# Kernel optimization log

Measured on AMD Instinct MI355X. Metric: run time of the kernel, lower is better.

## Reference

```python
import jax, jax.numpy as jnp
import numpy as np

H = 512      # hidden_size
V = 50257    # vocab_size
B = 64       # batch
T = 512      # sequence length


def setup_inputs() -> dict:
    key = jax.random.key(0)
    k1, k2, k3, k4 = jax.random.split(key, 4)
    # Parameters as constructed in HMM.__init__ (row-stochastic / log-normalized)
    alpha_exp = jax.nn.softmax(jax.random.normal(k1, (H, H), dtype=jnp.float32), axis=-1)
    beta = jax.nn.log_softmax(jax.random.normal(k2, (H, V), dtype=jnp.float32), axis=-1)
    gamma_exp = jax.nn.softmax(jax.random.normal(k3, (1, H), dtype=jnp.float32), axis=-1)
    input_ids = jax.random.randint(k4, (B, T), 0, V)
    return {"alpha_exp": alpha_exp, "beta": beta, "gamma_exp": gamma_exp, "input_ids": input_ids}


def _stable_mvm(log_W, log_x):
    # log-space matvec: log(W @ x) with max-shift stabilization (matches torch stable_mvm)
    x_max = jnp.max(log_x)
    x = jnp.exp(log_x - x_max)                       # (H,)
    w_max = jnp.max(log_W, axis=1, keepdims=True)    # (H,1)
    W = jnp.exp(log_W - w_max)                       # (H,H)
    z = W @ x                                        # (H,)
    return jnp.log(z) + x_max + jnp.squeeze(w_max, -1)


def reference(alpha_exp, beta, gamma_exp, input_ids):
    # HMM.compute_forward_probability
    logA_T = jnp.log(alpha_exp + 1e-12).T            # (H,H) transposed transition log-probs
    alpha0 = jnp.log(gamma_exp) + beta[:, input_ids[:, 0]].T   # (B,H)
    mvm = jax.vmap(_stable_mvm, in_axes=(None, 0))

    def step(alpha_prev, x_t):
        a = mvm(logA_T, alpha_prev) + beta[:, x_t].T  # (B,H)
        return a, None

    alpha_final, _ = jax.lax.scan(step, alpha0, input_ids[:, 1:].T)
    return alpha_final
```

## Files before the change

kernel.cpp:

```cpp
#include <hip/hip_runtime.h>
#include <hip/hip_bf16.h>

#define HH 512
#define VV 50257
#define TL 512
#define NT 512
#define DYN_LDS 98304

typedef __attribute__((ext_vector_type(4))) float floatx4;
typedef __attribute__((ext_vector_type(8))) int intx8;

__device__ __forceinline__ unsigned short f2bf(float f) {
  union { float f; unsigned int u; } v; v.f = f;
  unsigned int r = (v.u + 0x7fffu + ((v.u >> 16) & 1u)) >> 16;
  return (unsigned short)r;
}
__device__ __forceinline__ float bf2f(unsigned short h) {
  union { unsigned int u; float f; } v; v.u = ((unsigned int)h) << 16;
  return v.f;
}

__device__ __forceinline__ float wave_max_dpp(float x) {
  int xi = __builtin_bit_cast(int, x);
#define DPPSTEP(ctrl)                                                              \
  {                                                                                \
    int yi = __builtin_amdgcn_update_dpp(xi, xi, (ctrl), 0xf, 0xf, false);         \
    float a = __builtin_bit_cast(float, xi), b = __builtin_bit_cast(float, yi);    \
    xi = __builtin_bit_cast(int, fmaxf(a, b));                                     \
  }
  DPPSTEP(0xB1)
  DPPSTEP(0x4E)
  DPPSTEP(0x141)
  DPPSTEP(0x140)
  DPPSTEP(0x142)
  DPPSTEP(0x143)
#undef DPPSTEP
  return __builtin_bit_cast(float, __builtin_amdgcn_readlane(xi, 63));
}

__global__ void colmaxK(const float* __restrict__ A, float* __restrict__ cmax) {
  __shared__ float red[4][64];
  int x = threadIdx.x & 63;
  int y = threadIdx.x >> 6;
  int c = blockIdx.x * 64 + x;
  float m = -INFINITY;
  for (int j = y; j < HH; j += 4) m = fmaxf(m, A[j * HH + c]);
  red[y][x] = m;
  __syncthreads();
  if (y == 0)
    cmax[c] = fmaxf(fmaxf(red[0][x], red[1][x]), fmaxf(red[2][x], red[3][x])) + 1e-12f;
}

__global__ void buildWf8sK(const float* __restrict__ A, const float* __restrict__ cmax,
                           intx8* __restrict__ Wf8s) {
  int gid = blockIdx.x * 256 + threadIdx.x;
  int L = gid & 63, r = gid >> 6;
  int kk = r & 3, T = r >> 2;
  int n = T * 16 + (L & 15);
  int kbase = kk * 128 + (L >> 4) * 32;
  float inv = 1.0f / cmax[n];
  intx8 o;
#pragma unroll
  for (int d = 0; d < 8; ++d) {
    float v0 = (A[(kbase + 4 * d + 0) * HH + n] + 1e-12f) * inv;
    float v1 = (A[(kbase + 4 * d + 1) * HH + n] + 1e-12f) * inv;
    float v2 = (A[(kbase + 4 * d + 2) * HH + n] + 1e-12f) * inv;
    float v3 = (A[(kbase + 4 * d + 3) * HH + n] + 1e-12f) * inv;
    unsigned pk;
    asm("v_cvt_pk_fp8_f32 %0, %1, %2" : "=v"(pk) : "v"(v0), "v"(v1));
    asm("v_cvt_pk_fp8_f32 %0, %1, %2 op_sel:[0,0,1]" : "+v"(pk) : "v"(v2), "v"(v3));
    o[d] = (int)pk;
  }
  Wf8s[gid] = o;
}

__global__ void buildPtab(const float* __restrict__ beta, const float* __restrict__ cmax,
                          unsigned short* __restrict__ Ptab) {
  __shared__ float tile[32][33];
  int v0 = blockIdx.x * 32, h0 = blockIdx.y * 32;
  int tx = threadIdx.x, ty = threadIdx.y;
#pragma unroll
  for (int k = 0; k < 4; ++k) {
    int v = v0 + tx;
    if (v < VV) tile[ty + 8 * k][tx] = beta[(h0 + ty + 8 * k) * VV + v];
  }
  __syncthreads();
  float cm = cmax[h0 + tx];
#pragma unroll
  for (int k = 0; k < 4; ++k) {
    int v = v0 + ty + 8 * k;
    if (v < VV) Ptab[(long)v * HH + h0 + tx] = f2bf(__expf(tile[tx][ty + 8 * k]) * cm);
  }
}

__global__ __launch_bounds__(NT, 2) __attribute__((amdgpu_waves_per_eu(2, 2)))
void hmm_main(const intx8* __restrict__ Wf8s,
              const unsigned short* __restrict__ Ptab,
              const float* __restrict__ gamma,
              const float* __restrict__ cmax,
              const int* __restrict__ ids,
              float* __restrict__ out) {
  extern __shared__ char dls[];
  unsigned char* xbuf = (unsigned char*)dls;
  int* elds = (int*)(dls + 1024);
  int* ids_l = (int*)(dls + 1088);

  const int b = blockIdx.x, tid = threadIdx.x;
  const int w = tid >> 6, L = tid & 63;
  const int q = L >> 4;
  const long bT = (long)b * TL;

  ids_l[tid] = ids[bT + tid];

  intx8 wa[4][4];
#pragma unroll
  for (int tau = 0; tau < 4; ++tau)
#pragma unroll
    for (int kk = 0; kk < 4; ++kk)
      wa[tau][kk] = Wf8s[((4 * w + tau) * 4 + kk) * 64 + L];

  const int n = tid;
  float A = 0.f;

  {
    const int id0 = ids[bT];
    float u0 = gamma[n] * bf2f(Ptab[(long)id0 * HH + n]) / cmax[n];
    float m = wave_max_dpp(u0);
    int ebits = (__builtin_bit_cast(int, m) >> 23) & 0xFF;
    float nf = __builtin_bit_cast(float, (254 - ebits) << 23);
    float x0 = u0 * nf;
    unsigned pk;
    asm("v_cvt_pk_fp8_f32 %0, %1, %2" : "=v"(pk) : "v"(x0), "v"(x0));
    xbuf[n] = (unsigned char)(pk & 0xff);
    if (L == 0) elds[w] = ebits - 127;
    __syncthreads();
  }

  unsigned short pvc = Ptab[(long)ids_l[1] * HH + n];

  for (int t = 1; t < TL; ++t) {
    const int idn = ids_l[(t + 1 < TL) ? (t + 1) : t];
    const unsigned short pvn = Ptab[(long)idn * HH + n];

    const int pr = (t - 1) & 1;
    const unsigned char* xb = xbuf + pr * 512;

    int4 ea = *(const int4*)&elds[pr * 8];
    int4 eb = *(const int4*)&elds[pr * 8 + 4];
    int E = max(max(max(ea.x, ea.y), max(ea.z, ea.w)),
                max(max(eb.x, eb.y), max(eb.z, eb.w)));
    A += (float)E * 0.69314718056f;
    const int s0 = max(127 + ea.x - E, 0), s1 = max(127 + ea.y - E, 0);
    const int s2 = max(127 + ea.z - E, 0), s3 = max(127 + ea.w - E, 0);
    const int s4 = max(127 + eb.x - E, 0), s5 = max(127 + eb.y - E, 0);
    const int s6 = max(127 + eb.z - E, 0), s7 = max(127 + eb.w - E, 0);
    const int sa0 = s0 * 0x0101 + s1 * 0x01010000;
    const int sa1 = s2 * 0x0101 + s3 * 0x01010000;
    const int sa2 = s4 * 0x0101 + s5 * 0x01010000;
    const int sa3 = s6 * 0x0101 + s7 * 0x01010000;

    intx8 af0 = *(const intx8*)(xb + 0 * 128 + q * 32);
    intx8 af1 = *(const intx8*)(xb + 1 * 128 + q * 32);
    intx8 af2 = *(const intx8*)(xb + 2 * 128 + q * 32);
    intx8 af3 = *(const intx8*)(xb + 3 * 128 + q * 32);

    floatx4 acc[4];
#pragma unroll
    for (int tau = 0; tau < 4; ++tau) acc[tau] = (floatx4){0.f, 0.f, 0.f, 0.f};

    __builtin_amdgcn_s_setprio(1);
#pragma unroll
    for (int tau = 0; tau < 4; ++tau) {
      acc[tau] = __builtin_amdgcn_mfma_scale_f32_16x16x128_f8f6f4(
          af0, wa[tau][0], acc[tau], 0, 0, 0, sa0, 0, 0x7F7F7F7F);
      acc[tau] = __builtin_amdgcn_mfma_scale_f32_16x16x128_f8f6f4(
          af1, wa[tau][1], acc[tau], 0, 0, 0, sa1, 0, 0x7F7F7F7F);
      acc[tau] = __builtin_amdgcn_mfma_scale_f32_16x16x128_f8f6f4(
          af2, wa[tau][2], acc[tau], 0, 0, 0, sa2, 0, 0x7F7F7F7F);
      acc[tau] = __builtin_amdgcn_mfma_scale_f32_16x16x128_f8f6f4(
          af3, wa[tau][3], acc[tau], 0, 0, 0, sa3, 0, 0x7F7F7F7F);
    }
    __builtin_amdgcn_s_setprio(0);

    const float z = (q < 2) ? (q == 0 ? acc[0][0] : acc[1][0])
                            : (q == 2 ? acc[2][0] : acc[3][0]);
    const float un = z * bf2f(pvc);

    if (t == TL - 1) {
      out[(long)b * HH + n] = __logf(fmaxf(un, 1e-37f)) + A;
    } else {
      float m = wave_max_dpp(un);
      int ebits = (__builtin_bit_cast(int, m) >> 23) & 0xFF;
      float nf = __builtin_bit_cast(float, (254 - ebits) << 23);
      float x = un * nf;
      unsigned pk;
      asm("v_cvt_pk_fp8_f32 %0, %1, %2" : "=v"(pk) : "v"(x), "v"(x));
      xbuf[(t & 1) * 512 + n] = (unsigned char)(pk & 0xff);
      if (L == 0) elds[(t & 1) * 8 + w] = ebits - 127;
      asm volatile("s_waitcnt lgkmcnt(0)" ::: "memory");
      __builtin_amdgcn_s_barrier();
      __builtin_amdgcn_sched_barrier(0);
    }
    pvc = pvn;
  }
}

extern "C" void kernel_launch(void* const* d_in, const int* in_sizes, int n_in,
                              void* d_out, int out_size, void* d_ws, size_t ws_size,
                              hipStream_t stream) {
  const float* alpha_exp = (const float*)d_in[0];
  const float* beta = (const float*)d_in[1];
  const float* gamma = (const float*)d_in[2];
  const int* ids = (const int*)d_in[3];
  float* out = (float*)d_out;

  char* ws = (char*)d_ws;
  float* cmax = (float*)(ws + 0);
  intx8* Wf8s = (intx8*)(ws + 4096);
  unsigned short* Ptab = (unsigned short*)(ws + 528384);

  (void)hipFuncSetAttribute((const void*)hmm_main,
                            hipFuncAttributeMaxDynamicSharedMemorySize, DYN_LDS);

  colmaxK<<<8, 256, 0, stream>>>(alpha_exp, cmax);
  buildWf8sK<<<32, 256, 0, stream>>>(alpha_exp, cmax, Wf8s);
  dim3 gT((VV + 31) / 32, HH / 32), bTd(32, 8);
  buildPtab<<<gT, bTd, 0, stream>>>(beta, cmax, Ptab);

  hmm_main<<<64, NT, DYN_LDS, stream>>>(Wf8s, Ptab, gamma, cmax, ids, out);
}
```

Before: 623.9 us.

## Halve workgroup to four waves, each computing two output columns per step

Shrinks the per-batch workgroup from 8 waves to 4, so each wave holds twice as many fp8 weight tiles in registers (8x4 intx8) and each lane produces two hidden states per timestep. Per-wave exponents are stored as bytes and packed into one dword, which simplifies the scale computation. The intent is to cut barrier cost and cross-wave exponent reduction in the serial recurrence. In exchange, each wave issues twice as many MFMAs per step on the critical path, and register pressure rises sharply with one wave per EU.

```diff
diff --git a/kernel.cpp b/kernel.cpp
--- a/kernel.cpp
+++ b/kernel.cpp
@@ -4,7 +4,7 @@
 #define HH 512
 #define VV 50257
 #define TL 512
-#define NT 512
+#define NT 256
 #define DYN_LDS 98304
 
 typedef __attribute__((ext_vector_type(4))) float floatx4;
@@ -93,7 +93,7 @@
   }
 }
 
-__global__ __launch_bounds__(NT, 2) __attribute__((amdgpu_waves_per_eu(2, 2)))
+__global__ __launch_bounds__(NT, 1) __attribute__((amdgpu_waves_per_eu(1, 1)))
 void hmm_main(const intx8* __restrict__ Wf8s,
               const unsigned short* __restrict__ Ptab,
               const float* __restrict__ gamma,
@@ -102,106 +102,118 @@
               float* __restrict__ out) {
   extern __shared__ char dls[];
   unsigned char* xbuf = (unsigned char*)dls;
-  int* elds = (int*)(dls + 1024);
-  int* ids_l = (int*)(dls + 1088);
+  unsigned char* eldsb = (unsigned char*)(dls + 1024);
+  int* ids_l = (int*)(dls + 1040);
 
   const int b = blockIdx.x, tid = threadIdx.x;
   const int w = tid >> 6, L = tid & 63;
-  const int q = L >> 4;
+  const int q = L >> 4, l16 = L & 15;
   const long bT = (long)b * TL;
 
   ids_l[tid] = ids[bT + tid];
-
-  intx8 wa[4][4];
-#pragma unroll
-  for (int tau = 0; tau < 4; ++tau)
+  ids_l[tid + 256] = ids[bT + tid + 256];
+
+  intx8 wa[8][4];
+#pragma unroll
+  for (int tau = 0; tau < 8; ++tau)
 #pragma unroll
     for (int kk = 0; kk < 4; ++kk)
-      wa[tau][kk] = Wf8s[((4 * w + tau) * 4 + kk) * 64 + L];
-
-  const int n = tid;
+      wa[tau][kk] = Wf8s[((8 * w + tau) * 4 + kk) * 64 + L];
+
+  const int n0 = 128 * w + 32 * q + l16;
+  const int n1 = n0 + 16;
+
   float A = 0.f;
 
   {
     const int id0 = ids[bT];
-    float u0 = gamma[n] * bf2f(Ptab[(long)id0 * HH + n]) / cmax[n];
-    float m = wave_max_dpp(u0);
+    float u0 = gamma[n0] * bf2f(Ptab[(long)id0 * HH + n0]) / cmax[n0];
+    float u1 = gamma[n1] * bf2f(Ptab[(long)id0 * HH + n1]) / cmax[n1];
+    float m = wave_max_dpp(fmaxf(u0, u1));
     int ebits = (__builtin_bit_cast(int, m) >> 23) & 0xFF;
     float nf = __builtin_bit_cast(float, (254 - ebits) << 23);
-    float x0 = u0 * nf;
+    float x0 = u0 * nf, x1 = u1 * nf;
     unsigned pk;
-    asm("v_cvt_pk_fp8_f32 %0, %1, %2" : "=v"(pk) : "v"(x0), "v"(x0));
-    xbuf[n] = (unsigned char)(pk & 0xff);
-    if (L == 0) elds[w] = ebits - 127;
+    asm("v_cvt_pk_fp8_f32 %0, %1, %2" : "=v"(pk) : "v"(x0), "v"(x1));
+    xbuf[n0] = (unsigned char)(pk & 0xff);
+    xbuf[n1] = (unsigned char)((pk >> 8) & 0xff);
+    if (L == 0) eldsb[w] = (unsigned char)ebits;
     __syncthreads();
   }
 
-  unsigned short pvc = Ptab[(long)ids_l[1] * HH + n];
+  unsigned short pv0c = Ptab[(long)ids_l[1] * HH + n0];
+  unsigned short pv1c = Ptab[(long)ids_l[1] * HH + n1];
 
   for (int t = 1; t < TL; ++t) {
     const int idn = ids_l[(t + 1 < TL) ? (t + 1) : t];
-    const unsigned short pvn = Ptab[(long)idn * HH + n];
-
-    const int pr = (t - 1) & 1;
+    const unsigned short pv0n = Ptab[(long)idn * HH + n0];
+    const unsigned short pv1n = Ptab[(long)idn * HH + n1];
+
+    const int pr = (t - 1) & 1, pw = t & 1;
     const unsigned char* xb = xbuf + pr * 512;
 
-    int4 ea = *(const int4*)&elds[pr * 8];
-    int4 eb = *(const int4*)&elds[pr * 8 + 4];
-    int E = max(max(max(ea.x, ea.y), max(ea.z, ea.w)),
-                max(max(eb.x, eb.y), max(eb.z, eb.w)));
-    A += (float)E * 0.69314718056f;
-    const int s0 = max(127 + ea.x - E, 0), s1 = max(127 + ea.y - E, 0);
-    const int s2 = max(127 + ea.z - E, 0), s3 = max(127 + ea.w - E, 0);
-    const int s4 = max(127 + eb.x - E, 0), s5 = max(127 + eb.y - E, 0);
-    const int s6 = max(127 + eb.z - E, 0), s7 = max(127 + eb.w - E, 0);
-    const int sa0 = s0 * 0x0101 + s1 * 0x01010000;
-    const int sa1 = s2 * 0x0101 + s3 * 0x01010000;
-    const int sa2 = s4 * 0x0101 + s5 * 0x01010000;
-    const int sa3 = s6 * 0x0101 + s7 * 0x01010000;
-
-    intx8 af0 = *(const intx8*)(xb + 0 * 128 + q * 32);
-    intx8 af1 = *(const intx8*)(xb + 1 * 128 + q * 32);
-    intx8 af2 = *(const intx8*)(xb + 2 * 128 + q * 32);
-    intx8 af3 = *(const intx8*)(xb + 3 * 128 + q * 32);
-
-    floatx4 acc[4];
-#pragma unroll
-    for (int tau = 0; tau < 4; ++tau) acc[tau] = (floatx4){0.f, 0.f, 0.f, 0.f};
-
-    __builtin_amdgcn_s_setprio(1);
-#pragma unroll
-    for (int tau = 0; tau < 4; ++tau) {
-      acc[tau] = __builtin_amdgcn_mfma_scale_f32_16x16x128_f8f6f4(
-          af0, wa[tau][0], acc[tau], 0, 0, 0, sa0, 0, 0x7F7F7F7F);
-      acc[tau] = __builtin_amdgcn_mfma_scale_f32_16x16x128_f8f6f4(
-          af1, wa[tau][1], acc[tau], 0, 0, 0, sa1, 0, 0x7F7F7F7F);
-      acc[tau] = __builtin_amdgcn_mfma_scale_f32_16x16x128_f8f6f4(
-          af2, wa[tau][2], acc[tau], 0, 0, 0, sa2, 0, 0x7F7F7F7F);
-      acc[tau] = __builtin_amdgcn_mfma_scale_f32_16x16x128_f8f6f4(
-          af3, wa[tau][3], acc[tau], 0, 0, 0, sa3, 0, 0x7F7F7F7F);
-    }
-    __builtin_amdgcn_s_setprio(0);
-
-    const float z = (q < 2) ? (q == 0 ? acc[0][0] : acc[1][0])
-                            : (q == 2 ? acc[2][0] : acc[3][0]);
-    const float un = z * bf2f(pvc);
+    const unsigned edw = *(const unsigned*)(eldsb + pr * 4);
+    const int ub0 = edw & 0xff, ub1 = (edw >> 8) & 0xff;
+    const int ub2 = (edw >> 16) & 0xff, ub3 = edw >> 24;
+    const int mu = max(max(ub0, ub1), max(ub2, ub3));
+    A += (float)(mu - 127) * 0.69314718056f;
+    const unsigned sa0 = (unsigned)max(ub0 - mu + 127, 0) * 0x01010101u;
+    const unsigned sa1 = (unsigned)max(ub1 - mu + 127, 0) * 0x01010101u;
+    const unsigned sa2 = (unsigned)max(ub2 - mu + 127, 0) * 0x01010101u;
+    const unsigned sa3 = (unsigned)max(ub3 - mu + 127, 0) * 0x01010101u;
+
+    const intx8 af0 = *(const intx8*)(xb + 0 * 128 + q * 32);
+    const intx8 af1 = *(const intx8*)(xb + 1 * 128 + q * 32);
+    const intx8 af2 = *(const intx8*)(xb + 2 * 128 + q * 32);
+    const intx8 af3 = *(const intx8*)(xb + 3 * 128 + q * 32);
+
+    floatx4 acc[8];
+#pragma unroll
+    for (int tau = 0; tau < 8; ++tau) acc[tau] = (floatx4){0.f, 0.f, 0.f, 0.f};
+
+#pragma unroll
+    for (int tau = 0; tau < 8; ++tau)
+      acc[tau] = __builtin_amdgcn_mfma_scale_f32_16x16x128_f8f6f4(
+          af0, wa[tau][0], acc[tau], 0, 0, 0, (int)sa0, 0, 0x7F7F7F7F);
+#pragma unroll
+    for (int tau = 0; tau < 8; ++tau)
+      acc[tau] = __builtin_amdgcn_mfma_scale_f32_16x16x128_f8f6f4(
+          af1, wa[tau][1], acc[tau], 0, 0, 0, (int)sa1, 0, 0x7F7F7F7F);
+#pragma unroll
+    for (int tau = 0; tau < 8; ++tau)
+      acc[tau] = __builtin_amdgcn_mfma_scale_f32_16x16x128_f8f6f4(
+          af2, wa[tau][2], acc[tau], 0, 0, 0, (int)sa2, 0, 0x7F7F7F7F);
+#pragma unroll
+    for (int tau = 0; tau < 8; ++tau)
+      acc[tau] = __builtin_amdgcn_mfma_scale_f32_16x16x128_f8f6f4(
+          af3, wa[tau][3], acc[tau], 0, 0, 0, (int)sa3, 0, 0x7F7F7F7F);
+
+    const float z0 = (q < 2) ? (q == 0 ? acc[0][0] : acc[2][0])
+                             : (q == 2 ? acc[4][0] : acc[6][0]);
+    const float z1 = (q < 2) ? (q == 0 ? acc[1][0] : acc[3][0])
+                             : (q == 2 ? acc[5][0] : acc[7][0]);
+    const float un0 = z0 * bf2f(pv0c);
+    const float un1 = z1 * bf2f(pv1c);
 
     if (t == TL - 1) {
-      out[(long)b * HH + n] = __logf(fmaxf(un, 1e-37f)) + A;
+      out[(long)b * HH + n0] = __logf(fmaxf(un0, 1e-37f)) + A;
+      out[(long)b * HH + n1] = __logf(fmaxf(un1, 1e-37f)) + A;
     } else {
-      float m = wave_max_dpp(un);
+      float m = wave_max_dpp(fmaxf(un0, un1));
       int ebits = (__builtin_bit_cast(int, m) >> 23) & 0xFF;
       float nf = __builtin_bit_cast(float, (254 - ebits) << 23);
-      float x = un * nf;
+      float x0 = un0 * nf, x1 = un1 * nf;
       unsigned pk;
-      asm("v_cvt_pk_fp8_f32 %0, %1, %2" : "=v"(pk) : "v"(x), "v"(x));
-      xbuf[(t & 1) * 512 + n] = (unsigned char)(pk & 0xff);
-      if (L == 0) elds[(t & 1) * 8 + w] = ebits - 127;
+      asm("v_cvt_pk_fp8_f32 %0, %1, %2" : "=v"(pk) : "v"(x0), "v"(x1));
+      xbuf[pw * 512 + n0] = (unsigned char)(pk & 0xff);
+      xbuf[pw * 512 + n1] = (unsigned char)((pk >> 8) & 0xff);
+      if (L == 0) eldsb[pw * 4 + w] = (unsigned char)ebits;
       asm volatile("s_waitcnt lgkmcnt(0)" ::: "memory");
       __builtin_amdgcn_s_barrier();
       __builtin_amdgcn_sched_barrier(0);
     }
-    pvc = pvn;
+    pv0c = pv0n;
+    pv1c = pv1n;
   }
 }
 
```

New measurement: 619.5 us. About the same (-0.7%).
